# Optimization experiments

Measured on AMD Instinct MI355X. Metric: run time of the kernel, lower is better.

Reference implementation:

```python
import jax, jax.numpy as jnp
import numpy as np

D_MODEL = 1024
NUM_HEADS = 16
D_K = D_MODEL // NUM_HEADS


def setup_inputs() -> dict:
    key = jax.random.key(0)
    ks = jax.random.split(key, 11)
    B, S = 2, 2048
    scale = 1.0 / np.sqrt(D_MODEL)
    inp = {
        'q': jax.random.normal(ks[0], (B, S, D_MODEL), dtype=jnp.float32),
        'k': jax.random.normal(ks[1], (B, S, D_MODEL), dtype=jnp.float32),
        'v': jax.random.normal(ks[2], (B, S, D_MODEL), dtype=jnp.float32),
        'W_q': jax.random.normal(ks[3], (D_MODEL, D_MODEL), dtype=jnp.float32) * scale,
        'b_q': jnp.zeros((D_MODEL,), dtype=jnp.float32),
        'W_k': jax.random.normal(ks[4], (D_MODEL, D_MODEL), dtype=jnp.float32) * scale,
        'b_k': jnp.zeros((D_MODEL,), dtype=jnp.float32),
        'W_v': jax.random.normal(ks[5], (D_MODEL, D_MODEL), dtype=jnp.float32) * scale,
        'b_v': jnp.zeros((D_MODEL,), dtype=jnp.float32),
        'W_o': jax.random.normal(ks[6], (D_MODEL, D_MODEL), dtype=jnp.float32) * scale,
        'b_o': jnp.zeros((D_MODEL,), dtype=jnp.float32),
    }
    return inp


def _split_heads(x):
    # [B, S, D] -> [B, H, S, d_k]
    B, S, _ = x.shape
    return x.reshape(B, S, NUM_HEADS, D_K).transpose(0, 2, 1, 3)


def reference(q, k, v, W_q, b_q, W_k, b_k, W_v, b_v, W_o, b_o):
    # Linear projections (torch Linear: x @ W.T + b)
    qh = _split_heads(q @ W_q.T + b_q)  # [B,H,S,dk]
    kh = _split_heads(k @ W_k.T + b_k)
    vh = _split_heads(v @ W_v.T + b_v)
    scores = jnp.einsum('bhsd,bhtd->bhst', qh, kh) / jnp.sqrt(
        jnp.asarray(D_K, dtype=qh.dtype))  # [B,H,S,S]
    probs = jax.nn.softmax(scores, axis=-1)
    attn = jnp.einsum('bhst,bhtd->bhsd', probs, vh)  # [B,H,S,dk]
    B, H, S, dk = attn.shape
    combined = attn.transpose(0, 2, 1, 3).reshape(B, S, H * dk)  # [B,S,D]
    return combined @ W_o.T + b_o
```

## Files before the change

kernel.cpp:

```cpp
#include <hip/hip_runtime.h>
#include <hip/hip_bf16.h>

typedef __bf16 bf16;
typedef __attribute__((ext_vector_type(4))) __bf16 bf16x4;
typedef __attribute__((ext_vector_type(8))) __bf16 bf16x8;
typedef __attribute__((ext_vector_type(4))) float f32x4;
typedef __attribute__((ext_vector_type(4))) short short4v;

#define AS1C(p) ((const __attribute__((address_space(1))) void*)(p))
#define AS3(p)  ((__attribute__((address_space(3))) void*)(p))

static constexpr int B_ = 2, S_ = 2048, DM = 1024, H_ = 16, DK = 64;
static constexpr int M_ = B_ * S_;
static constexpr int NW = DM * DM;
static constexpr float QSCL = 0.125f * 1.44269504088896340736f;

__device__ __forceinline__ float fast_exp2(float x) {
#if __has_builtin(__builtin_amdgcn_exp2f)
  return __builtin_amdgcn_exp2f(x);
#else
  return exp2f(x);
#endif
}

__device__ __forceinline__ f32x4 mfma_pv(bf16x4 a, bf16x4 b, f32x4 c) {
#if __has_builtin(__builtin_amdgcn_mfma_f32_16x16x16_bf16)
  return __builtin_amdgcn_mfma_f32_16x16x16_bf16(a, b, c, 0, 0, 0);
#else
  union U { bf16x4 h; short4v s; };
  U ua; ua.h = a;
  U ub; ub.h = b;
  return __builtin_amdgcn_mfma_f32_16x16x16bf16_1k(ua.s, ub.s, c, 0, 0, 0);
#endif
}

__global__ __launch_bounds__(256) void cast_all(
    const float* Wq, const float* Wk, const float* Wv, const float* Wo,
    const float* q, const float* k, const float* v,
    bf16* Wc, bf16* WoC, bf16* qc, bf16* kc, bf16* vc)
{
  const int id = blockIdx.x;
  const float* in;
  bf16* out;
  float s = 1.0f;
  int base;
  if (id < 2048) {
    const int z = id >> 9;
    base = id & 511;
    in  = z == 0 ? Wq : (z == 1 ? Wk : (z == 2 ? Wv : Wo));
    out = z < 3 ? (Wc + (size_t)z * NW) : WoC;
    if (z == 0) s = QSCL;
  } else {
    const int z = (id - 2048) >> 11;
    base = (id - 2048) & 2047;
    in  = z == 0 ? q : (z == 1 ? k : v);
    out = z == 0 ? qc : (z == 1 ? kc : vc);
  }
  const size_t i = ((size_t)base * 256 + threadIdx.x) * 8;
  f32x4 a = *(const f32x4*)(in + i);
  f32x4 b2 = *(const f32x4*)(in + i + 4);
  bf16x8 o;
#pragma unroll
  for (int j = 0; j < 4; ++j) { o[j] = (bf16)(a[j] * s); o[4 + j] = (bf16)(b2[j] * s); }
  *(bf16x8*)(out + i) = o;
}

__global__ __launch_bounds__(256, 3) void gemm_qkv_b(
    const bf16* __restrict__ qc, const bf16* __restrict__ kc,
    const bf16* __restrict__ vc, const bf16* __restrict__ Wc,
    const float* b0, const float* b1, const float* b2,
    bf16* C0, bf16* C1, bf16* C2, int M, int N, int K)
{
  const int id = blockIdx.x;
  const int z  = id >> 8;
  const int r  = id & 255;
  const int by = r & 31;
  const int bx = r >> 5;
  const bf16* A = z == 0 ? qc : (z == 1 ? kc : vc);
  const float* bias = z == 0 ? b0 : (z == 1 ? b1 : b2);
  const float bscale = z == 0 ? QSCL : 1.0f;
  const bf16* W = Wc + (size_t)z * NW;
  bf16* Cout = z == 0 ? C0 : (z == 1 ? C1 : C2);
  const bool transv = (z == 2);

  __shared__ bf16 As[2 * 128 * 32];
  __shared__ bf16 Bs[2 * 128 * 32];

  const int tid  = threadIdx.x;
  const int wave = tid >> 6, lane = tid & 63;
  const int quad = lane >> 4, l16 = lane & 15;
  const int wm = wave >> 1, wn = wave & 1;
  const int row0 = by * 128;
  const int col0 = bx * 128;

  const int srow  = lane >> 2;
  const int skcol = (lane & 3) * 8;

  f32x4 acc[4][4] = {};

  for (int k0 = 0; k0 < K; k0 += 64) {
    __syncthreads();
#pragma unroll
    for (int hf = 0; hf < 2; ++hf)
#pragma unroll
      for (int c = wave; c < 8; c += 4)
        __builtin_amdgcn_global_load_lds(
            AS1C(A + (size_t)(row0 + c * 16 + srow) * K + k0 + hf * 32 + skcol),
            AS3(As + hf * 4096 + c * 512), 16, 0, 0);
#pragma unroll
    for (int hf = 0; hf < 2; ++hf)
#pragma unroll
      for (int i = 0; i < 2; ++i) {
        const int c = wave * 2 + i;
        __builtin_amdgcn_global_load_lds(
            AS1C(W + (size_t)(col0 + c * 16 + srow) * K + k0 + hf * 32 + skcol),
            AS3(Bs + hf * 4096 + c * 512), 16, 0, 0);
      }
    __syncthreads();

#pragma unroll
    for (int hf = 0; hf < 2; ++hf) {
      bf16x8 a[4], bfr[4];
#pragma unroll
      for (int i = 0; i < 4; ++i)
        a[i] = *(const bf16x8*)(As + hf * 4096 + (wm * 64 + i * 16 + l16) * 32 + quad * 8);
#pragma unroll
      for (int j = 0; j < 4; ++j)
        bfr[j] = *(const bf16x8*)(Bs + hf * 4096 + (wn * 64 + j * 16 + l16) * 32 + quad * 8);
#pragma unroll
      for (int i = 0; i < 4; ++i)
#pragma unroll
        for (int j = 0; j < 4; ++j)
          acc[i][j] = __builtin_amdgcn_mfma_f32_16x16x32_bf16(a[i], bfr[j], acc[i][j], 0, 0, 0);
    }
  }

#pragma unroll
  for (int j = 0; j < 4; ++j) {
    const int col = col0 + wn * 64 + j * 16 + l16;
    const float bv = bias[col] * bscale;
    if (transv) {
      const int hh = col >> 6, dd = col & 63;
#pragma unroll
      for (int i = 0; i < 4; ++i) {
        const int row = row0 + wm * 64 + i * 16 + quad * 4;
        const int bb2 = row >> 11, tok = row & 2047;
        bf16x4 o;
#pragma unroll
        for (int r2 = 0; r2 < 4; ++r2) o[r2] = (bf16)(acc[i][j][r2] + bv);
        *(bf16x4*)(Cout + (((size_t)bb2 * H_ + hh) * DK + dd) * S_ + tok) = o;
      }
    } else {
#pragma unroll
      for (int i = 0; i < 4; ++i)
#pragma unroll
        for (int r2 = 0; r2 < 4; ++r2) {
          const int row = row0 + wm * 64 + i * 16 + quad * 4 + r2;
          Cout[(size_t)row * N + col] = (bf16)(acc[i][j][r2] + bv);
        }
    }
  }
}

__global__ __launch_bounds__(256) void gemm_qkv_f(
    const float* A0, const float* A1, const float* A2,
    const bf16* __restrict__ Wc,
    const float* b0, const float* b1, const float* b2,
    bf16* C0, bf16* C1, bf16* C2, int M, int N, int K)
{
  const int id = blockIdx.x;
  const int z  = id >> 8;
  const int r  = id & 255;
  const int by = r & 31;
  const int bx = r >> 5;
  const float* A = z == 0 ? A0 : (z == 1 ? A1 : A2);
  const float* bias = z == 0 ? b0 : (z == 1 ? b1 : b2);
  const float bscale = z == 0 ? QSCL : 1.0f;
  const bf16* W = Wc + (size_t)z * NW;
  bf16* Cout = z == 0 ? C0 : (z == 1 ? C1 : C2);
  const bool transv = (z == 2);

  __shared__ bf16 As[2 * 128 * 32];
  __shared__ bf16 Bs[2 * 128 * 32];

  const int tid  = threadIdx.x;
  const int wave = tid >> 6, lane = tid & 63;
  const int quad = lane >> 4, l16 = lane & 15;
  const int wm = wave >> 1, wn = wave & 1;
  const int row0 = by * 128;
  const int col0 = bx * 128;

  const int srow  = lane >> 2;
  const int skcol = (lane & 3) * 8;

  const int arow  = (tid >> 1) & 127;
  const int ak16  = (tid & 1) * 16;
  const float* agp = A + (size_t)(row0 + arow) * K + ak16;
  f32x4 pre[8];
#pragma unroll
  for (int hf = 0; hf < 2; ++hf)
#pragma unroll
    for (int c = 0; c < 4; ++c)
      pre[hf * 4 + c] = *(const f32x4*)(agp + hf * 32 + c * 4);

  f32x4 acc[4][4] = {};

  for (int k0 = 0; k0 < K; k0 += 64) {
    __syncthreads();
#pragma unroll
    for (int hf = 0; hf < 2; ++hf) {
      bf16x8 w0, w1;
#pragma unroll
      for (int j = 0; j < 4; ++j) {
        w0[j]     = (bf16)pre[hf * 4 + 0][j];
        w0[4 + j] = (bf16)pre[hf * 4 + 1][j];
        w1[j]     = (bf16)pre[hf * 4 + 2][j];
        w1[4 + j] = (bf16)pre[hf * 4 + 3][j];
      }
      bf16* dst = As + hf * 4096 + arow * 32 + ak16;
      *(bf16x8*)dst = w0;
      *(bf16x8*)(dst + 8) = w1;
    }
#pragma unroll
    for (int hf = 0; hf < 2; ++hf)
#pragma unroll
      for (int i = 0; i < 2; ++i) {
        const int c = wave * 2 + i;
        __builtin_amdgcn_global_load_lds(
            AS1C(W + (size_t)(col0 + c * 16 + srow) * K + k0 + hf * 32 + skcol),
            AS3(Bs + hf * 4096 + c * 512), 16, 0, 0);
      }
    __syncthreads();

    if (k0 + 64 < K) {
#pragma unroll
      for (int hf = 0; hf < 2; ++hf)
#pragma unroll
        for (int c = 0; c < 4; ++c)
          pre[hf * 4 + c] = *(const f32x4*)(agp + k0 + 64 + hf * 32 + c * 4);
    }

#pragma unroll
    for (int hf = 0; hf < 2; ++hf) {
      bf16x8 a[4], bfr[4];
#pragma unroll
      for (int i = 0; i < 4; ++i)
        a[i] = *(const bf16x8*)(As + hf * 4096 + (wm * 64 + i * 16 + l16) * 32 + quad * 8);
#pragma unroll
      for (int j = 0; j < 4; ++j)
        bfr[j] = *(const bf16x8*)(Bs + hf * 4096 + (wn * 64 + j * 16 + l16) * 32 + quad * 8);
#pragma unroll
      for (int i = 0; i < 4; ++i)
#pragma unroll
        for (int j = 0; j < 4; ++j)
          acc[i][j] = __builtin_amdgcn_mfma_f32_16x16x32_bf16(a[i], bfr[j], acc[i][j], 0, 0, 0);
    }
  }

#pragma unroll
  for (int j = 0; j < 4; ++j) {
    const int col = col0 + wn * 64 + j * 16 + l16;
    const float bv = bias[col] * bscale;
    if (transv) {
      const int hh = col >> 6, dd = col & 63;
#pragma unroll
      for (int i = 0; i < 4; ++i) {
        const int row = row0 + wm * 64 + i * 16 + quad * 4;
        const int bb2 = row >> 11, tok = row & 2047;
        bf16x4 o;
#pragma unroll
        for (int r2 = 0; r2 < 4; ++r2) o[r2] = (bf16)(acc[i][j][r2] + bv);
        *(bf16x4*)(Cout + (((size_t)bb2 * H_ + hh) * DK + dd) * S_ + tok) = o;
      }
    } else {
#pragma unroll
      for (int i = 0; i < 4; ++i)
#pragma unroll
        for (int r2 = 0; r2 < 4; ++r2) {
          const int row = row0 + wm * 64 + i * 16 + quad * 4 + r2;
          Cout[(size_t)row * N + col] = (bf16)(acc[i][j][r2] + bv);
        }
    }
  }
}

__global__ __launch_bounds__(256, 2) void gemm_out(
    const bf16* __restrict__ Ain, const bf16* __restrict__ W,
    const float* __restrict__ bias, float* __restrict__ Cout,
    int M, int N, int K)
{
  const int id = blockIdx.x;
  const int by = id & 63;
  const int bx = id >> 6;

  __shared__ bf16 As0[2 * 64 * 32], As1[2 * 64 * 32];
  __shared__ bf16 Bs0[2 * 128 * 32], Bs1[2 * 128 * 32];

  const int tid  = threadIdx.x;
  const int wave = tid >> 6, lane = tid & 63;
  const int quad = lane >> 4, l16 = lane & 15;
  const int wm = wave >> 1, wn = wave & 1;
  const int row0 = by * 64;
  const int col0 = bx * 128;

  const int srow  = lane >> 2;
  const int skcol = (lane & 3) * 8;

  auto stage_A = [&](int k0, bf16* dst) {
#pragma unroll
    for (int hf = 0; hf < 2; ++hf)
      __builtin_amdgcn_global_load_lds(
          AS1C(Ain + (size_t)(row0 + wave * 16 + srow) * K + k0 + hf * 32 + skcol),
          AS3(dst + hf * 2048 + wave * 512), 16, 0, 0);
  };
  auto stage_W = [&](int k0, bf16* dst) {
#pragma unroll
    for (int hf = 0; hf < 2; ++hf)
#pragma unroll
      for (int i = 0; i < 2; ++i) {
        const int c = wave * 2 + i;
        __builtin_amdgcn_global_load_lds(
            AS1C(W + (size_t)(col0 + c * 16 + srow) * K + k0 + hf * 32 + skcol),
            AS3(dst + hf * 4096 + c * 512), 16, 0, 0);
      }
  };

  f32x4 acc[2][4] = {};

  auto mfma_tile = [&](const bf16* Ab, const bf16* Bb) {
#pragma unroll
    for (int hf = 0; hf < 2; ++hf) {
      bf16x8 a[2], bfr[4];
#pragma unroll
      for (int i = 0; i < 2; ++i)
        a[i] = *(const bf16x8*)(Ab + hf * 2048 + (wm * 32 + i * 16 + l16) * 32 + quad * 8);
#pragma unroll
      for (int j = 0; j < 4; ++j)
        bfr[j] = *(const bf16x8*)(Bb + hf * 4096 + (wn * 64 + j * 16 + l16) * 32 + quad * 8);
#pragma unroll
      for (int i = 0; i < 2; ++i)
#pragma unroll
        for (int j = 0; j < 4; ++j)
          acc[i][j] = __builtin_amdgcn_mfma_f32_16x16x32_bf16(a[i], bfr[j], acc[i][j], 0, 0, 0);
    }
  };

  const int NK = K / 64;
  stage_A(0, As0);
  stage_W(0, Bs0);
  __syncthreads();

  for (int t2 = 0; t2 < NK / 2; ++t2) {
    const int t = t2 * 2;
    if (t + 1 < NK) { stage_A((t + 1) * 64, As1); stage_W((t + 1) * 64, Bs1); }
    mfma_tile(As0, Bs0);
    __syncthreads();
    if (t + 2 < NK) { stage_A((t + 2) * 64, As0); stage_W((t + 2) * 64, Bs0); }
    mfma_tile(As1, Bs1);
    __syncthreads();
  }

#pragma unroll
  for (int j = 0; j < 4; ++j) {
    const int col = col0 + wn * 64 + j * 16 + l16;
    const float bv = bias[col];
#pragma unroll
    for (int i = 0; i < 2; ++i)
#pragma unroll
      for (int r = 0; r < 4; ++r) {
        const int row = row0 + wm * 32 + i * 16 + quad * 4 + r;
        Cout[(size_t)row * N + col] = acc[i][j][r] + bv;
      }
  }
}

__global__ __launch_bounds__(256, 2) void attn_kernel(
    const bf16* Q, const bf16* __restrict__ Kb,
    const bf16* __restrict__ Vtg, bf16* O)
{
  __shared__ bf16 Kt[2 * 64 * 64];
  __shared__ bf16 Vt[2 * 64 * 64];

  const int tid  = threadIdx.x;
  const int wave = tid >> 6, lane = tid & 63;
  const int quad = lane >> 4, l16 = lane & 15;
  const int id = blockIdx.x;
  const int hb = id & 31;
  const int h = hb & 15, b = hb >> 4;
  const int qt = id >> 5;
  const int qA = qt * 128 + wave * 32;
  const size_t base  = (size_t)b * S_ * DM + (size_t)h * DK;
  const size_t baseV = ((size_t)b * H_ + h) * DK * S_;

  bf16x8 qf[2][2];
#pragma unroll
  for (int f = 0; f < 2; ++f)
#pragma unroll
    for (int kt = 0; kt < 2; ++kt)
      qf[f][kt] = *(const bf16x8*)(Q + base + (size_t)(qA + f * 16 + l16) * DM + kt * 32 + quad * 8);

  const bool kside = (wave < 2);
  const int srow  = kside ? (tid >> 1) : ((tid - 128) >> 1);
  const int shalf = tid & 1;
  const bf16* gp = kside
      ? (Kb + base + (size_t)srow * DM + shalf * 32)
      : (Vtg + baseV + (size_t)srow * S_ + shalf * 32);
  const size_t gstep = kside ? (size_t)64 * DM : 64;
  char* sb = (char*)(kside ? (void*)Kt : (void*)Vt) + srow * 128;
  const int sw_s = (srow & 7) << 4;

  bf16x8 st[4];
#pragma unroll
  for (int c = 0; c < 4; ++c) st[c] = *(const bf16x8*)(gp + c * 8);
  gp += gstep;
#pragma unroll
  for (int c = 0; c < 4; ++c)
    *(bf16x8*)(sb + ((shalf * 64 + c * 16) ^ sw_s)) = st[c];
#pragma unroll
  for (int c = 0; c < 4; ++c) st[c] = *(const bf16x8*)(gp + c * 8);
  gp += gstep;

  f32x4 lacc[2] = {};
  f32x4 accO[2][4] = {};
  const int sw = (l16 & 7) << 4;

  __syncthreads();

  constexpr int NIT = S_ / 64;
  for (int it = 0; it < NIT; ++it) {
    const int cur = it & 1, nxt = cur ^ 1;
    const char* Kc = (const char*)Kt + cur * 8192;
    const char* Vc = (const char*)Vt + cur * 8192;

    f32x4 sc[2][4];
#pragma unroll
    for (int ct = 0; ct < 4; ++ct) {
      const char* kp = Kc + (ct * 16 + l16) * 128;
      const bf16x8 kf0 = *(const bf16x8*)(kp + ((quad * 16) ^ sw));
      const bf16x8 kf1 = *(const bf16x8*)(kp + ((64 + quad * 16) ^ sw));
#pragma unroll
      for (int f = 0; f < 2; ++f) {
        f32x4 a = {0.f, 0.f, 0.f, 0.f};
        a = __builtin_amdgcn_mfma_f32_16x16x32_bf16(kf0, qf[f][0], a, 0, 0, 0);
        a = __builtin_amdgcn_mfma_f32_16x16x32_bf16(kf1, qf[f][1], a, 0, 0, 0);
        sc[f][ct] = a;
      }
    }

    if (it + 1 < NIT) {
#pragma unroll
      for (int c = 0; c < 4; ++c)
        *(bf16x8*)(sb + nxt * 8192 + ((shalf * 64 + c * 16) ^ sw_s)) = st[c];
      if (it + 2 < NIT) {
#pragma unroll
        for (int c = 0; c < 4; ++c) st[c] = *(const bf16x8*)(gp + c * 8);
        gp += gstep;
      }
    }

    bf16x4 pk[2][4];
#pragma unroll
    for (int f = 0; f < 2; ++f)
#pragma unroll
      for (int ct = 0; ct < 4; ++ct)
#pragma unroll
        for (int r = 0; r < 4; ++r) {
          const float p = fast_exp2(sc[f][ct][r]);
          lacc[f][r] += p;
          pk[f][ct][r] = (bf16)p;
        }

#pragma unroll
    for (int dt = 0; dt < 4; ++dt) {
      const char* vp = Vc + (dt * 16 + l16) * 128;
#pragma unroll
      for (int ct = 0; ct < 4; ++ct) {
        const bf16x4 vf = *(const bf16x4*)(vp + ((ct * 32 + quad * 8) ^ sw));
#pragma unroll
        for (int f = 0; f < 2; ++f)
          accO[f][dt] = mfma_pv(vf, pk[f][ct], accO[f][dt]);
      }
    }

    __syncthreads();
  }

#pragma unroll
  for (int f = 0; f < 2; ++f) {
    float l_s = (lacc[f][0] + lacc[f][1]) + (lacc[f][2] + lacc[f][3]);
    l_s += __shfl_xor(l_s, 16, 64);
    l_s += __shfl_xor(l_s, 32, 64);
    const float inv = 1.0f / l_s;
#pragma unroll
    for (int dt = 0; dt < 4; ++dt) {
      bf16x4 o;
#pragma unroll
      for (int r = 0; r < 4; ++r) o[r] = (bf16)(accO[f][dt][r] * inv);
      *(bf16x4*)(O + base + (size_t)(qA + f * 16 + l16) * DM + dt * 16 + quad * 4) = o;
    }
  }
}

extern "C" void kernel_launch(void* const* d_in, const int* in_sizes, int n_in,
                              void* d_out, int out_size, void* d_ws, size_t ws_size,
                              hipStream_t stream) {
  (void)in_sizes; (void)n_in; (void)out_size;
  const float* q  = (const float*)d_in[0];
  const float* k  = (const float*)d_in[1];
  const float* v  = (const float*)d_in[2];
  const float* Wq = (const float*)d_in[3];
  const float* bq = (const float*)d_in[4];
  const float* Wk = (const float*)d_in[5];
  const float* bk = (const float*)d_in[6];
  const float* Wv = (const float*)d_in[7];
  const float* bvv= (const float*)d_in[8];
  const float* Wo = (const float*)d_in[9];
  const float* bo = (const float*)d_in[10];
  float* out = (float*)d_out;

  char* ws = (char*)d_ws;
  const size_t MB = 1024 * 1024;
  bf16* Qb  = (bf16*)(ws);
  bf16* Kbf = (bf16*)(ws + 8 * MB);
  bf16* Vtg = (bf16*)(ws + 16 * MB);
  bf16* Wc  = (bf16*)(ws + 24 * MB);
  bf16* WoC = (bf16*)(ws + 30 * MB);
  bf16* qc  = (bf16*)(ws + 32 * MB);
  bf16* kc  = (bf16*)(ws + 40 * MB);
  bf16* vc  = (bf16*)(ws + 48 * MB);
  bf16* Ab  = Qb;

  const bool big = ws_size >= 60 * MB;
  dim3 bb(256, 1, 1);

  cast_all<<<dim3(big ? 8192 : 2048, 1, 1), bb, 0, stream>>>(
      Wq, Wk, Wv, Wo, q, k, v, Wc, WoC, qc, kc, vc);

  if (big) {
    gemm_qkv_b<<<dim3(768, 1, 1), bb, 0, stream>>>(
        qc, kc, vc, Wc, bq, bk, bvv, Qb, Kbf, Vtg, M_, DM, DM);
  } else {
    gemm_qkv_f<<<dim3(768, 1, 1), bb, 0, stream>>>(
        q, k, v, Wc, bq, bk, bvv, Qb, Kbf, Vtg, M_, DM, DM);
  }

  attn_kernel<<<dim3(512, 1, 1), bb, 0, stream>>>(Qb, Kbf, Vtg, Ab);

  gemm_out<<<dim3(512, 1, 1), bb, 0, stream>>>(Ab, WoC, bo, out, M_, DM, DM);
}
```

Baseline: 209.3 us.

## Stage K/V tiles via direct global-to-LDS loads and permute V layout

Replaces the register-staged K/V prefetch in the attention kernel with __builtin_amdgcn_global_load_lds asynchronous copies into the double-buffered LDS tiles, using an XOR swizzle on the source offset. The QKV projection epilogue now writes V^T with a token permutation within each 32-token group, so the PV loop can load one 16-byte bf16x8 and split it into two bf16x4 MFMA operands instead of issuing two 8-byte LDS reads. This is meant to cut VGPR pressure and LDS read instructions. The risk is that the layout permutation must match exactly across kernels, and the direct-to-LDS loads still have to be correctly fenced by the existing barrier.

```diff
diff --git a/kernel.cpp b/kernel.cpp
--- a/kernel.cpp
+++ b/kernel.cpp
@@ -32,6 +32,11 @@
   U ub; ub.h = b;
   return __builtin_amdgcn_mfma_f32_16x16x16bf16_1k(ua.s, ub.s, c, 0, 0, 0);
 #endif
+}
+
+__device__ __forceinline__ int vperm_tok(int tok) {
+  const int t5 = tok & 31;
+  return (tok & ~31) | (((t5 >> 2) & 3) * 8) | (((t5 >> 4) & 1) * 4);
 }
 
 __global__ __launch_bounds__(256) void cast_all(
@@ -145,10 +150,11 @@
       for (int i = 0; i < 4; ++i) {
         const int row = row0 + wm * 64 + i * 16 + quad * 4;
         const int bb2 = row >> 11, tok = row & 2047;
+        const int tokp = vperm_tok(tok);
         bf16x4 o;
 #pragma unroll
         for (int r2 = 0; r2 < 4; ++r2) o[r2] = (bf16)(acc[i][j][r2] + bv);
-        *(bf16x4*)(Cout + (((size_t)bb2 * H_ + hh) * DK + dd) * S_ + tok) = o;
+        *(bf16x4*)(Cout + (((size_t)bb2 * H_ + hh) * DK + dd) * S_ + tokp) = o;
       }
     } else {
 #pragma unroll
@@ -267,10 +273,11 @@
       for (int i = 0; i < 4; ++i) {
         const int row = row0 + wm * 64 + i * 16 + quad * 4;
         const int bb2 = row >> 11, tok = row & 2047;
+        const int tokp = vperm_tok(tok);
         bf16x4 o;
 #pragma unroll
         for (int r2 = 0; r2 < 4; ++r2) o[r2] = (bf16)(acc[i][j][r2] + bv);
-        *(bf16x4*)(Cout + (((size_t)bb2 * H_ + hh) * DK + dd) * S_ + tok) = o;
+        *(bf16x4*)(Cout + (((size_t)bb2 * H_ + hh) * DK + dd) * S_ + tokp) = o;
       }
     } else {
 #pragma unroll
@@ -399,31 +406,29 @@
     for (int kt = 0; kt < 2; ++kt)
       qf[f][kt] = *(const bf16x8*)(Q + base + (size_t)(qA + f * 16 + l16) * DM + kt * 32 + quad * 8);
 
-  const bool kside = (wave < 2);
-  const int srow  = kside ? (tid >> 1) : ((tid - 128) >> 1);
-  const int shalf = tid & 1;
-  const bf16* gp = kside
-      ? (Kb + base + (size_t)srow * DM + shalf * 32)
-      : (Vtg + baseV + (size_t)srow * S_ + shalf * 32);
-  const size_t gstep = kside ? (size_t)64 * DM : 64;
-  char* sb = (char*)(kside ? (void*)Kt : (void*)Vt) + srow * 128;
-  const int sw_s = (srow & 7) << 4;
-
-  bf16x8 st[4];
-#pragma unroll
-  for (int c = 0; c < 4; ++c) st[c] = *(const bf16x8*)(gp + c * 8);
-  gp += gstep;
-#pragma unroll
-  for (int c = 0; c < 4; ++c)
-    *(bf16x8*)(sb + ((shalf * 64 + c * 16) ^ sw_s)) = st[c];
-#pragma unroll
-  for (int c = 0; c < 4; ++c) st[c] = *(const bf16x8*)(gp + c * 8);
-  gp += gstep;
+  const int r8 = lane >> 3;
+  const int so = ((lane & 7) ^ r8) << 3;
+  const bf16* gK = Kb + base;
+  const bf16* gV = Vtg + baseV;
+
+  auto stage = [&](int t, int buf) {
+#pragma unroll
+    for (int o8 = 0; o8 < 16; o8 += 8) {
+      const int row = wave * 16 + o8 + r8;
+      __builtin_amdgcn_global_load_lds(
+          AS1C(gK + (size_t)(t * 64 + row) * DM + so),
+          AS3(Kt + buf * 4096 + (wave * 16 + o8) * 64), 16, 0, 0);
+      __builtin_amdgcn_global_load_lds(
+          AS1C(gV + (size_t)row * S_ + t * 64 + so),
+          AS3(Vt + buf * 4096 + (wave * 16 + o8) * 64), 16, 0, 0);
+    }
+  };
 
   f32x4 lacc[2] = {};
   f32x4 accO[2][4] = {};
   const int sw = (l16 & 7) << 4;
 
+  stage(0, 0);
   __syncthreads();
 
   constexpr int NIT = S_ / 64;
@@ -447,16 +452,7 @@
       }
     }
 
-    if (it + 1 < NIT) {
-#pragma unroll
-      for (int c = 0; c < 4; ++c)
-        *(bf16x8*)(sb + nxt * 8192 + ((shalf * 64 + c * 16) ^ sw_s)) = st[c];
-      if (it + 2 < NIT) {
-#pragma unroll
-        for (int c = 0; c < 4; ++c) st[c] = *(const bf16x8*)(gp + c * 8);
-        gp += gstep;
-      }
-    }
+    if (it + 1 < NIT) stage(it + 1, nxt);
 
     bf16x4 pk[2][4];
 #pragma unroll
@@ -474,11 +470,15 @@
     for (int dt = 0; dt < 4; ++dt) {
       const char* vp = Vc + (dt * 16 + l16) * 128;
 #pragma unroll
-      for (int ct = 0; ct < 4; ++ct) {
-        const bf16x4 vf = *(const bf16x4*)(vp + ((ct * 32 + quad * 8) ^ sw));
-#pragma unroll
-        for (int f = 0; f < 2; ++f)
-          accO[f][dt] = mfma_pv(vf, pk[f][ct], accO[f][dt]);
+      for (int g = 0; g < 2; ++g) {
+        const bf16x8 v8 = *(const bf16x8*)(vp + ((g * 64 + quad * 16) ^ sw));
+        const bf16x4 vlo = __builtin_shufflevector(v8, v8, 0, 1, 2, 3);
+        const bf16x4 vhi = __builtin_shufflevector(v8, v8, 4, 5, 6, 7);
+#pragma unroll
+        for (int f = 0; f < 2; ++f) {
+          accO[f][dt] = mfma_pv(vlo, pk[f][2 * g],     accO[f][dt]);
+          accO[f][dt] = mfma_pv(vhi, pk[f][2 * g + 1], accO[f][dt]);
+        }
       }
     }
 
```

New measurement: 209.6 us. About the same (+0.1%).

## Shrink output GEMM tile to 64x64 and drop double-buffering for more blocks

Applied to the files above, without the earlier changes.

Output projection GEMM now uses 64x64 tiles instead of 64x128 and launches 1024 blocks instead of 512, with launch bounds raised to four blocks per SM. The double-buffered LDS pipeline is replaced by a single buffer with two barriers per K step. The goal is more parallelism and occupancy across CUs for this small GEMM. In exchange, each block reuses less data, global traffic for A rises, and load latency is no longer overlapped within a block.

```diff
diff --git a/kernel.cpp b/kernel.cpp
--- a/kernel.cpp
+++ b/kernel.cpp
@@ -284,7 +284,7 @@
   }
 }
 
-__global__ __launch_bounds__(256, 2) void gemm_out(
+__global__ __launch_bounds__(256, 4) void gemm_out(
     const bf16* __restrict__ Ain, const bf16* __restrict__ W,
     const float* __restrict__ bias, float* __restrict__ Cout,
     int M, int N, int K)
@@ -293,76 +293,54 @@
   const int by = id & 63;
   const int bx = id >> 6;
 
-  __shared__ bf16 As0[2 * 64 * 32], As1[2 * 64 * 32];
-  __shared__ bf16 Bs0[2 * 128 * 32], Bs1[2 * 128 * 32];
+  __shared__ bf16 As[2 * 64 * 32];
+  __shared__ bf16 Bs[2 * 64 * 32];
 
   const int tid  = threadIdx.x;
   const int wave = tid >> 6, lane = tid & 63;
   const int quad = lane >> 4, l16 = lane & 15;
   const int wm = wave >> 1, wn = wave & 1;
   const int row0 = by * 64;
-  const int col0 = bx * 128;
+  const int col0 = bx * 64;
 
   const int srow  = lane >> 2;
   const int skcol = (lane & 3) * 8;
 
-  auto stage_A = [&](int k0, bf16* dst) {
-#pragma unroll
-    for (int hf = 0; hf < 2; ++hf)
+  f32x4 acc[2][2] = {};
+
+  for (int k0 = 0; k0 < K; k0 += 64) {
+    __syncthreads();
+#pragma unroll
+    for (int hf = 0; hf < 2; ++hf) {
       __builtin_amdgcn_global_load_lds(
           AS1C(Ain + (size_t)(row0 + wave * 16 + srow) * K + k0 + hf * 32 + skcol),
-          AS3(dst + hf * 2048 + wave * 512), 16, 0, 0);
-  };
-  auto stage_W = [&](int k0, bf16* dst) {
-#pragma unroll
-    for (int hf = 0; hf < 2; ++hf)
-#pragma unroll
-      for (int i = 0; i < 2; ++i) {
-        const int c = wave * 2 + i;
-        __builtin_amdgcn_global_load_lds(
-            AS1C(W + (size_t)(col0 + c * 16 + srow) * K + k0 + hf * 32 + skcol),
-            AS3(dst + hf * 4096 + c * 512), 16, 0, 0);
-      }
-  };
-
-  f32x4 acc[2][4] = {};
-
-  auto mfma_tile = [&](const bf16* Ab, const bf16* Bb) {
+          AS3(As + hf * 2048 + wave * 512), 16, 0, 0);
+      __builtin_amdgcn_global_load_lds(
+          AS1C(W + (size_t)(col0 + wave * 16 + srow) * K + k0 + hf * 32 + skcol),
+          AS3(Bs + hf * 2048 + wave * 512), 16, 0, 0);
+    }
+    __syncthreads();
+
 #pragma unroll
     for (int hf = 0; hf < 2; ++hf) {
-      bf16x8 a[2], bfr[4];
+      bf16x8 a[2], bfr[2];
 #pragma unroll
       for (int i = 0; i < 2; ++i)
-        a[i] = *(const bf16x8*)(Ab + hf * 2048 + (wm * 32 + i * 16 + l16) * 32 + quad * 8);
-#pragma unroll
-      for (int j = 0; j < 4; ++j)
-        bfr[j] = *(const bf16x8*)(Bb + hf * 4096 + (wn * 64 + j * 16 + l16) * 32 + quad * 8);
+        a[i] = *(const bf16x8*)(As + hf * 2048 + (wm * 32 + i * 16 + l16) * 32 + quad * 8);
+#pragma unroll
+      for (int j = 0; j < 2; ++j)
+        bfr[j] = *(const bf16x8*)(Bs + hf * 2048 + (wn * 32 + j * 16 + l16) * 32 + quad * 8);
 #pragma unroll
       for (int i = 0; i < 2; ++i)
 #pragma unroll
-        for (int j = 0; j < 4; ++j)
+        for (int j = 0; j < 2; ++j)
           acc[i][j] = __builtin_amdgcn_mfma_f32_16x16x32_bf16(a[i], bfr[j], acc[i][j], 0, 0, 0);
     }
-  };
-
-  const int NK = K / 64;
-  stage_A(0, As0);
-  stage_W(0, Bs0);
-  __syncthreads();
-
-  for (int t2 = 0; t2 < NK / 2; ++t2) {
-    const int t = t2 * 2;
-    if (t + 1 < NK) { stage_A((t + 1) * 64, As1); stage_W((t + 1) * 64, Bs1); }
-    mfma_tile(As0, Bs0);
-    __syncthreads();
-    if (t + 2 < NK) { stage_A((t + 2) * 64, As0); stage_W((t + 2) * 64, Bs0); }
-    mfma_tile(As1, Bs1);
-    __syncthreads();
-  }
-
-#pragma unroll
-  for (int j = 0; j < 4; ++j) {
-    const int col = col0 + wn * 64 + j * 16 + l16;
+  }
+
+#pragma unroll
+  for (int j = 0; j < 2; ++j) {
+    const int col = col0 + wn * 32 + j * 16 + l16;
     const float bv = bias[col];
 #pragma unroll
     for (int i = 0; i < 2; ++i)
@@ -546,5 +524,5 @@
 
   attn_kernel<<<dim3(512, 1, 1), bb, 0, stream>>>(Qb, Kbf, Vtg, Ab);
 
-  gemm_out<<<dim3(512, 1, 1), bb, 0, stream>>>(Ab, WoC, bo, out, M_, DM, DM);
-}
+  gemm_out<<<dim3(1024, 1, 1), bb, 0, stream>>>(Ab, WoC, bo, out, M_, DM, DM);
+}
```

Result: no change. 209.0 us (-0.2%).
